# Kernel optimization log

Hardware: AMD Instinct MI355X
Metric: run time of the kernel (lower is better)

Reference implementation:

```python
import jax, jax.numpy as jnp
import numpy as np

N_PTS = 2_000_000
N_VOX = 500_000
N_EMB = 1_000_000
EMBED_DIM = 16


def _interp_offset():
    # 8 corners of the unit cube, same order as torch.meshgrid([0,1]*3) -> reshape(-1,3)
    o = jnp.array([0.0, 1.0], dtype=jnp.float32)
    return jnp.stack(jnp.meshgrid(o, o, o, indexing='ij'), axis=-1).reshape(-1, 3)  # [8,3]


def setup_inputs() -> dict:
    key = jax.random.key(0)
    k1, k2, k3, k4, k5 = jax.random.split(key, 5)
    pts = jax.random.uniform(k1, (N_PTS, 3), dtype=jnp.float32)
    p2v_idx = jax.random.randint(k2, (N_PTS,), 0, N_VOX, dtype=jnp.int64 if jax.config.jax_enable_x64 else jnp.int32)
    embeddings = jax.random.normal(k3, (N_EMB, EMBED_DIM), dtype=jnp.float32) * (EMBED_DIM ** -0.5)
    center_points = jax.random.uniform(k4, (N_VOX, 3), dtype=jnp.float32)
    center2corner = jax.random.randint(k5, (N_VOX, 8), 0, N_EMB, dtype=jnp.int64 if jax.config.jax_enable_x64 else jnp.int32)
    voxel_size = jnp.ones((1,), dtype=jnp.float32)
    return {"pts": pts, "p2v_idx": p2v_idx, "embeddings": embeddings,
            "center_points": center_points, "center2corner": center2corner,
            "voxel_size": voxel_size}


def reference(pts, p2v_idx, embeddings, center_points, center2corner, voxel_size):
    offset = _interp_offset()                      # [8,3]
    cp = center_points[p2v_idx]                    # [N,3]   gather voxel centers
    cidx = center2corner[p2v_idx]                  # [N,8]   gather corner indices
    emb = embeddings[cidx]                         # [N,8,D] gather corner embeddings
    # relative position inside voxel, in [0,1]
    p = (pts - cp) / voxel_size + 0.5              # [N,3]
    p = p[:, None, :]                              # [N,1,3]
    # trilinear weights: prod over xyz of (p if corner==1 else 1-p)
    r = jnp.prod(p * offset + (1.0 - p) * (1.0 - offset), axis=-1)  # [N,8]
    return jnp.einsum('nc,ncd->nd', r, emb)        # [N,D]
```

## Files before the change

### kernel.cpp

```cpp
#include <hip/hip_runtime.h>


typedef float v4f __attribute__((ext_vector_type(4)));

__global__ void k_zero(unsigned* __restrict__ hist, int n) {
    int i = blockIdx.x * blockDim.x + threadIdx.x;
    if (i < n) hist[i] = 0u;
}

__global__ __launch_bounds__(256) void k_hist_rank(const int* __restrict__ p2v,
                                                   unsigned* __restrict__ hist,
                                                   unsigned* __restrict__ rank, int N) {
    const int base = (blockIdx.x * blockDim.x + threadIdx.x) * 8;
    if (base + 7 < N) {
        const int4 a = *(const int4*)(p2v + base);
        const int4 b = *(const int4*)(p2v + base + 4);
        const unsigned r0 = atomicAdd(&hist[a.x], 1u);
        const unsigned r1 = atomicAdd(&hist[a.y], 1u);
        const unsigned r2 = atomicAdd(&hist[a.z], 1u);
        const unsigned r3 = atomicAdd(&hist[a.w], 1u);
        const unsigned r4 = atomicAdd(&hist[b.x], 1u);
        const unsigned r5 = atomicAdd(&hist[b.y], 1u);
        const unsigned r6 = atomicAdd(&hist[b.z], 1u);
        const unsigned r7 = atomicAdd(&hist[b.w], 1u);
        uint4 o0; o0.x = r0; o0.y = r1; o0.z = r2; o0.w = r3;
        uint4 o1; o1.x = r4; o1.y = r5; o1.z = r6; o1.w = r7;
        *(uint4*)(rank + base)     = o0;
        *(uint4*)(rank + base + 4) = o1;
    } else {
        for (int k = 0; k < 8; ++k)
            if (base + k < N) rank[base + k] = atomicAdd(&hist[p2v[base + k]], 1u);
    }
}

__global__ __launch_bounds__(256) void k_scan_blocks(unsigned* __restrict__ hist,
                                                     unsigned* __restrict__ bsums, int nbins) {
    __shared__ unsigned tsum[256];
    const int tid = threadIdx.x;
    const int i0 = blockIdx.x * 1024 + tid * 4;
    unsigned v[4]; unsigned s = 0;
    #pragma unroll
    for (int k = 0; k < 4; ++k) {
        unsigned c = (i0 + k < nbins) ? hist[i0 + k] : 0u;
        v[k] = s; s += c;
    }
    tsum[tid] = s; __syncthreads();
    for (int off = 1; off < 256; off <<= 1) {
        unsigned x = tsum[tid];
        unsigned y = (tid >= off) ? tsum[tid - off] : 0u;
        __syncthreads();
        tsum[tid] = x + y;
        __syncthreads();
    }
    unsigned prefix = (tid > 0) ? tsum[tid - 1] : 0u;
    #pragma unroll
    for (int k = 0; k < 4; ++k) {
        if (i0 + k < nbins) hist[i0 + k] = prefix + v[k];
    }
    if (tid == 255) bsums[blockIdx.x] = tsum[255];
}

__global__ __launch_bounds__(256) void k_scan_sums(unsigned* __restrict__ bsums, int nb) {
    __shared__ unsigned tsum[256];
    const int tid = threadIdx.x;
    const int i0 = tid * 4;
    unsigned v[4]; unsigned s = 0;
    #pragma unroll
    for (int k = 0; k < 4; ++k) {
        unsigned c = (i0 + k < nb) ? bsums[i0 + k] : 0u;
        v[k] = s; s += c;
    }
    tsum[tid] = s; __syncthreads();
    for (int off = 1; off < 256; off <<= 1) {
        unsigned x = tsum[tid];
        unsigned y = (tid >= off) ? tsum[tid - off] : 0u;
        __syncthreads();
        tsum[tid] = x + y;
        __syncthreads();
    }
    unsigned prefix = (tid > 0) ? tsum[tid - 1] : 0u;
    #pragma unroll
    for (int k = 0; k < 4; ++k) {
        if (i0 + k < nb) bsums[i0 + k] = prefix + v[k];
    }
}

__global__ __launch_bounds__(256) void k_place(
    const float* __restrict__ pts,
    const int*   __restrict__ p2v,
    const unsigned* __restrict__ rank,
    const unsigned* __restrict__ hist,
    const unsigned* __restrict__ bsums,
    unsigned* __restrict__ vsort,
    v4f*      __restrict__ rec,
    int N)
{
    const int base = (blockIdx.x * blockDim.x + threadIdx.x) * 4;
    if (base + 3 < N) {
        const int4  v4r = *(const int4*)(p2v + base);
        const uint4 r4  = *(const uint4*)(rank + base);
        const v4f* p4 = (const v4f*)pts;
        const size_t f0i = (size_t)(3 * (base >> 2));
        const v4f f0 = p4[f0i];
        const v4f f1 = p4[f0i + 1];
        const v4f f2 = p4[f0i + 2];

        const unsigned pos0 = hist[v4r.x] + bsums[((unsigned)v4r.x) >> 10] + r4.x;
        const unsigned pos1 = hist[v4r.y] + bsums[((unsigned)v4r.y) >> 10] + r4.y;
        const unsigned pos2 = hist[v4r.z] + bsums[((unsigned)v4r.z) >> 10] + r4.z;
        const unsigned pos3 = hist[v4r.w] + bsums[((unsigned)v4r.w) >> 10] + r4.w;

        vsort[pos0] = (unsigned)v4r.x;
        vsort[pos1] = (unsigned)v4r.y;
        vsort[pos2] = (unsigned)v4r.z;
        vsort[pos3] = (unsigned)v4r.w;

        v4f a;
        a.x = f0.x; a.y = f0.y; a.z = f0.z; a.w = __int_as_float(base + 0);
        rec[pos0] = a;
        a.x = f0.w; a.y = f1.x; a.z = f1.y; a.w = __int_as_float(base + 1);
        rec[pos1] = a;
        a.x = f1.z; a.y = f1.w; a.z = f2.x; a.w = __int_as_float(base + 2);
        rec[pos2] = a;
        a.x = f2.y; a.y = f2.z; a.z = f2.w; a.w = __int_as_float(base + 3);
        rec[pos3] = a;
    } else {
        for (int k = 0; k < 4; ++k) {
            const int i = base + k;
            if (i >= N) break;
            const int v = p2v[i];
            const unsigned pos = hist[v] + bsums[((unsigned)v) >> 10] + rank[i];
            vsort[pos] = (unsigned)v;
            v4f r;
            r.x = pts[3 * (size_t)i + 0];
            r.y = pts[3 * (size_t)i + 1];
            r.z = pts[3 * (size_t)i + 2];
            r.w = __int_as_float(i);
            rec[pos] = r;
        }
    }
}

__global__ __launch_bounds__(256) void k_main(
    const unsigned* __restrict__ vsort, const v4f* __restrict__ rec,
    const float* __restrict__ emb,
    const float* __restrict__ cp,
    const int*   __restrict__ c2c,
    const float* __restrict__ vox,
    float*       __restrict__ out,
    int N)
{
    const int t = blockIdx.x * blockDim.x + threadIdx.x;
    const int n = t >> 2;
    const int q = t & 3;
    if (n >= N) return;

    const unsigned v = vsort[n];
    const v4f r = rec[n];
    const int orig = __float_as_int(r.w);

    const int4* c4 = (const int4*)(c2c + 8 * (size_t)v);
    const int4 ci0 = c4[0];
    const int4 ci1 = c4[1];
    const int cidx[8] = {ci0.x, ci0.y, ci0.z, ci0.w, ci1.x, ci1.y, ci1.z, ci1.w};

    v4f e[8];
    #pragma unroll
    for (int c = 0; c < 8; ++c) {
        e[c] = *(const v4f*)(emb + 16 * (size_t)cidx[c] + 4 * q);
    }

    const float inv_vs = 1.0f / vox[0];
    const float* cpp = cp + 3 * (size_t)v;
    const float px = (r.x - cpp[0]) * inv_vs + 0.5f;
    const float py = (r.y - cpp[1]) * inv_vs + 0.5f;
    const float pz = (r.z - cpp[2]) * inv_vs + 0.5f;
    const float wx[2] = {1.0f - px, px};
    const float wy[2] = {1.0f - py, py};
    const float wz[2] = {1.0f - pz, pz};

    v4f acc = (v4f)(0.0f);
    #pragma unroll
    for (int c = 0; c < 8; ++c) {
        const float w = wx[(c >> 2) & 1] * wy[(c >> 1) & 1] * wz[c & 1];
        acc.x = fmaf(w, e[c].x, acc.x);
        acc.y = fmaf(w, e[c].y, acc.y);
        acc.z = fmaf(w, e[c].z, acc.z);
        acc.w = fmaf(w, e[c].w, acc.w);
    }

    __builtin_nontemporal_store(acc, (v4f*)(out + 16 * (size_t)orig + 4 * q));
}

__global__ __launch_bounds__(256) void k_direct(
    const float* __restrict__ pts, const int* __restrict__ p2v,
    const float* __restrict__ emb, const float* __restrict__ cp,
    const int* __restrict__ c2c, const float* __restrict__ vox,
    float* __restrict__ out, int N)
{
    const int t = blockIdx.x * blockDim.x + threadIdx.x;
    const int n = t >> 2, q = t & 3;
    if (n >= N) return;
    const int v = p2v[n];
    const int4* c4 = (const int4*)(c2c + 8 * (size_t)v);
    const int4 ci0 = c4[0], ci1 = c4[1];
    const int cidx[8] = {ci0.x, ci0.y, ci0.z, ci0.w, ci1.x, ci1.y, ci1.z, ci1.w};
    v4f e[8];
    #pragma unroll
    for (int c = 0; c < 8; ++c) e[c] = *(const v4f*)(emb + 16 * (size_t)cidx[c] + 4 * q);
    const float inv_vs = 1.0f / vox[0];
    const float* pp = pts + 3 * (size_t)n;
    const float* cpp = cp + 3 * (size_t)v;
    const float px = (pp[0] - cpp[0]) * inv_vs + 0.5f;
    const float py = (pp[1] - cpp[1]) * inv_vs + 0.5f;
    const float pz = (pp[2] - cpp[2]) * inv_vs + 0.5f;
    const float wx[2] = {1.0f - px, px};
    const float wy[2] = {1.0f - py, py};
    const float wz[2] = {1.0f - pz, pz};
    v4f acc = (v4f)(0.0f);
    #pragma unroll
    for (int c = 0; c < 8; ++c) {
        const float w = wx[(c >> 2) & 1] * wy[(c >> 1) & 1] * wz[c & 1];
        acc.x = fmaf(w, e[c].x, acc.x); acc.y = fmaf(w, e[c].y, acc.y);
        acc.z = fmaf(w, e[c].z, acc.z); acc.w = fmaf(w, e[c].w, acc.w);
    }
    __builtin_nontemporal_store(acc, (v4f*)(out + 4 * (size_t)t));
}

extern "C" void kernel_launch(void* const* d_in, const int* in_sizes, int n_in,
                              void* d_out, int out_size, void* d_ws, size_t ws_size,
                              hipStream_t stream) {
    const float* pts = (const float*)d_in[0];
    const int*   p2v = (const int*)d_in[1];
    const float* emb = (const float*)d_in[2];
    const float* cp  = (const float*)d_in[3];
    const int*   c2c = (const int*)d_in[4];
    const float* vox = (const float*)d_in[5];
    float*       out = (float*)d_out;

    const int N  = in_sizes[1];
    const int NV = in_sizes[4] / 8;

    const size_t off_hist  = 0;
    const size_t off_bsums = 2u * 1024u * 1024u;
    const size_t off_rank  = 4u * 1024u * 1024u;
    const size_t off_vsort = 12u * 1024u * 1024u;
    const size_t off_rec   = 20u * 1024u * 1024u;
    const size_t need = off_rec + (size_t)N * 16u;

    if (ws_size < need) {
        const int block = 256;
        const long long threads = 4LL * N;
        k_direct<<<(int)((threads + block - 1) / block), block, 0, stream>>>(
            pts, p2v, emb, cp, c2c, vox, out, N);
        return;
    }

    unsigned* hist  = (unsigned*)((char*)d_ws + off_hist);
    unsigned* bsums = (unsigned*)((char*)d_ws + off_bsums);
    unsigned* rank  = (unsigned*)((char*)d_ws + off_rank);
    unsigned* vsort = (unsigned*)((char*)d_ws + off_vsort);
    v4f*      rec   = (v4f*)((char*)d_ws + off_rec);

    const int block = 256;
    const int nscan = (NV + 1023) / 1024;

    k_zero<<<(NV + block - 1) / block, block, 0, stream>>>(hist, NV);
    k_hist_rank<<<(N + block * 8 - 1) / (block * 8), block, 0, stream>>>(p2v, hist, rank, N);
    k_scan_blocks<<<nscan, 256, 0, stream>>>(hist, bsums, NV);
    k_scan_sums<<<1, 256, 0, stream>>>(bsums, nscan);
    k_place<<<(N + block * 4 - 1) / (block * 4), block, 0, stream>>>(
        pts, p2v, rank, hist, bsums, vsort, rec, N);

    const long long threads = 4LL * N;
    k_main<<<(int)((threads + block - 1) / block), block, 0, stream>>>(
        vsort, rec, emb, cp, c2c, vox, out, N);
}
```

Baseline: 458.5 us.

## Privatize voxel histogram per XCD to keep atomics local to each L2

The histogram used for the counting sort is replicated once per XCD, read via the XCC_ID hardware register. Atomics use workgroup scope on the XCD-local copy, and the XCD id is packed into the top bits of the rank. The scan interleaves the per-XCD counts to build per-copy bases, and placement decodes the tag. This aims to avoid cross-XCD coherence traffic on global atomics, at the cost of zeroing and scanning eight times more histogram memory and relying on workgroup-scope atomics staying coherent within an XCD's L2.

New measurement: 477.4 us. +4.1%, slower.

```diff
diff --git a/kernel.cpp b/kernel.cpp
--- a/kernel.cpp
+++ b/kernel.cpp
@@ -2,6 +2,7 @@
 
 
 typedef float v4f __attribute__((ext_vector_type(4)));
+#define NXCD 8
 
 __global__ void k_zero(unsigned* __restrict__ hist, int n) {
     int i = blockIdx.x * blockDim.x + threadIdx.x;
@@ -10,26 +11,35 @@
 
 __global__ __launch_bounds__(256) void k_hist_rank(const int* __restrict__ p2v,
                                                    unsigned* __restrict__ hist,
-                                                   unsigned* __restrict__ rank, int N) {
+                                                   unsigned* __restrict__ rank,
+                                                   int N, int NV) {
+    unsigned xcc;
+    asm volatile("s_getreg_b32 %0, hwreg(HW_REG_XCC_ID)" : "=s"(xcc));
+    xcc &= (NXCD - 1);
+    unsigned* __restrict__ hx = hist + (size_t)xcc * (size_t)NV;
+    const unsigned xtag = xcc << 28;
+
     const int base = (blockIdx.x * blockDim.x + threadIdx.x) * 8;
     if (base + 7 < N) {
         const int4 a = *(const int4*)(p2v + base);
         const int4 b = *(const int4*)(p2v + base + 4);
-        const unsigned r0 = atomicAdd(&hist[a.x], 1u);
-        const unsigned r1 = atomicAdd(&hist[a.y], 1u);
-        const unsigned r2 = atomicAdd(&hist[a.z], 1u);
-        const unsigned r3 = atomicAdd(&hist[a.w], 1u);
-        const unsigned r4 = atomicAdd(&hist[b.x], 1u);
-        const unsigned r5 = atomicAdd(&hist[b.y], 1u);
-        const unsigned r6 = atomicAdd(&hist[b.z], 1u);
-        const unsigned r7 = atomicAdd(&hist[b.w], 1u);
-        uint4 o0; o0.x = r0; o0.y = r1; o0.z = r2; o0.w = r3;
-        uint4 o1; o1.x = r4; o1.y = r5; o1.z = r6; o1.w = r7;
+        const unsigned r0 = __hip_atomic_fetch_add(&hx[a.x], 1u, __ATOMIC_RELAXED, __HIP_MEMORY_SCOPE_WORKGROUP);
+        const unsigned r1 = __hip_atomic_fetch_add(&hx[a.y], 1u, __ATOMIC_RELAXED, __HIP_MEMORY_SCOPE_WORKGROUP);
+        const unsigned r2 = __hip_atomic_fetch_add(&hx[a.z], 1u, __ATOMIC_RELAXED, __HIP_MEMORY_SCOPE_WORKGROUP);
+        const unsigned r3 = __hip_atomic_fetch_add(&hx[a.w], 1u, __ATOMIC_RELAXED, __HIP_MEMORY_SCOPE_WORKGROUP);
+        const unsigned r4 = __hip_atomic_fetch_add(&hx[b.x], 1u, __ATOMIC_RELAXED, __HIP_MEMORY_SCOPE_WORKGROUP);
+        const unsigned r5 = __hip_atomic_fetch_add(&hx[b.y], 1u, __ATOMIC_RELAXED, __HIP_MEMORY_SCOPE_WORKGROUP);
+        const unsigned r6 = __hip_atomic_fetch_add(&hx[b.z], 1u, __ATOMIC_RELAXED, __HIP_MEMORY_SCOPE_WORKGROUP);
+        const unsigned r7 = __hip_atomic_fetch_add(&hx[b.w], 1u, __ATOMIC_RELAXED, __HIP_MEMORY_SCOPE_WORKGROUP);
+        uint4 o0; o0.x = r0 | xtag; o0.y = r1 | xtag; o0.z = r2 | xtag; o0.w = r3 | xtag;
+        uint4 o1; o1.x = r4 | xtag; o1.y = r5 | xtag; o1.z = r6 | xtag; o1.w = r7 | xtag;
         *(uint4*)(rank + base)     = o0;
         *(uint4*)(rank + base + 4) = o1;
     } else {
         for (int k = 0; k < 8; ++k)
-            if (base + k < N) rank[base + k] = atomicAdd(&hist[p2v[base + k]], 1u);
+            if (base + k < N)
+                rank[base + k] = xtag | __hip_atomic_fetch_add(&hx[p2v[base + k]], 1u,
+                                        __ATOMIC_RELAXED, __HIP_MEMORY_SCOPE_WORKGROUP);
     }
 }
 
@@ -38,11 +48,28 @@
     __shared__ unsigned tsum[256];
     const int tid = threadIdx.x;
     const int i0 = blockIdx.x * 1024 + tid * 4;
-    unsigned v[4]; unsigned s = 0;
+    const bool full = (i0 + 3 < nbins);
+
+    unsigned h[NXCD][4];
+    #pragma unroll
+    for (int x = 0; x < NXCD; ++x) {
+        const unsigned* hp = hist + (size_t)x * (size_t)nbins;
+        if (full) {
+            const uint4 t = *(const uint4*)(hp + i0);
+            h[x][0] = t.x; h[x][1] = t.y; h[x][2] = t.z; h[x][3] = t.w;
+        } else {
+            #pragma unroll
+            for (int k = 0; k < 4; ++k) h[x][k] = (i0 + k < nbins) ? hp[i0 + k] : 0u;
+        }
+    }
+
+    unsigned vloc[4]; unsigned s = 0;
     #pragma unroll
     for (int k = 0; k < 4; ++k) {
-        unsigned c = (i0 + k < nbins) ? hist[i0 + k] : 0u;
-        v[k] = s; s += c;
+        unsigned t = 0;
+        #pragma unroll
+        for (int x = 0; x < NXCD; ++x) t += h[x][k];
+        vloc[k] = s; s += t;
     }
     tsum[tid] = s; __syncthreads();
     for (int off = 1; off < 256; off <<= 1) {
@@ -52,10 +79,25 @@
         tsum[tid] = x + y;
         __syncthreads();
     }
-    unsigned prefix = (tid > 0) ? tsum[tid - 1] : 0u;
+    const unsigned prefix = (tid > 0) ? tsum[tid - 1] : 0u;
+
+    unsigned basev[NXCD][4];
     #pragma unroll
     for (int k = 0; k < 4; ++k) {
-        if (i0 + k < nbins) hist[i0 + k] = prefix + v[k];
+        unsigned b = prefix + vloc[k];
+        #pragma unroll
+        for (int x = 0; x < NXCD; ++x) { basev[x][k] = b; b += h[x][k]; }
+    }
+    #pragma unroll
+    for (int x = 0; x < NXCD; ++x) {
+        unsigned* hp = hist + (size_t)x * (size_t)nbins;
+        if (full) {
+            uint4 o; o.x = basev[x][0]; o.y = basev[x][1]; o.z = basev[x][2]; o.w = basev[x][3];
+            *(uint4*)(hp + i0) = o;
+        } else {
+            #pragma unroll
+            for (int k = 0; k < 4; ++k) if (i0 + k < nbins) hp[i0 + k] = basev[x][k];
+        }
     }
     if (tid == 255) bsums[blockIdx.x] = tsum[255];
 }
@@ -93,7 +135,7 @@
     const unsigned* __restrict__ bsums,
     unsigned* __restrict__ vsort,
     v4f*      __restrict__ rec,
-    int N)
+    int N, int NV)
 {
     const int base = (blockIdx.x * blockDim.x + threadIdx.x) * 4;
     if (base + 3 < N) {
@@ -105,10 +147,14 @@
         const v4f f1 = p4[f0i + 1];
         const v4f f2 = p4[f0i + 2];
 
-        const unsigned pos0 = hist[v4r.x] + bsums[((unsigned)v4r.x) >> 10] + r4.x;
-        const unsigned pos1 = hist[v4r.y] + bsums[((unsigned)v4r.y) >> 10] + r4.y;
-        const unsigned pos2 = hist[v4r.z] + bsums[((unsigned)v4r.z) >> 10] + r4.z;
-        const unsigned pos3 = hist[v4r.w] + bsums[((unsigned)v4r.w) >> 10] + r4.w;
+        const unsigned pos0 = hist[(size_t)(r4.x >> 28) * NV + (unsigned)v4r.x]
+                              + bsums[((unsigned)v4r.x) >> 10] + (r4.x & 0x0FFFFFFFu);
+        const unsigned pos1 = hist[(size_t)(r4.y >> 28) * NV + (unsigned)v4r.y]
+                              + bsums[((unsigned)v4r.y) >> 10] + (r4.y & 0x0FFFFFFFu);
+        const unsigned pos2 = hist[(size_t)(r4.z >> 28) * NV + (unsigned)v4r.z]
+                              + bsums[((unsigned)v4r.z) >> 10] + (r4.z & 0x0FFFFFFFu);
+        const unsigned pos3 = hist[(size_t)(r4.w >> 28) * NV + (unsigned)v4r.w]
+                              + bsums[((unsigned)v4r.w) >> 10] + (r4.w & 0x0FFFFFFFu);
 
         vsort[pos0] = (unsigned)v4r.x;
         vsort[pos1] = (unsigned)v4r.y;
@@ -129,7 +175,9 @@
             const int i = base + k;
             if (i >= N) break;
             const int v = p2v[i];
-            const unsigned pos = hist[v] + bsums[((unsigned)v) >> 10] + rank[i];
+            const unsigned rr = rank[i];
+            const unsigned pos = hist[(size_t)(rr >> 28) * NV + (unsigned)v]
+                                 + bsums[((unsigned)v) >> 10] + (rr & 0x0FFFFFFFu);
             vsort[pos] = (unsigned)v;
             v4f r;
             r.x = pts[3 * (size_t)i + 0];
@@ -241,11 +289,12 @@
     const int N  = in_sizes[1];
     const int NV = in_sizes[4] / 8;
 
+    const size_t MB = 1024u * 1024u;
     const size_t off_hist  = 0;
-    const size_t off_bsums = 2u * 1024u * 1024u;
-    const size_t off_rank  = 4u * 1024u * 1024u;
-    const size_t off_vsort = 12u * 1024u * 1024u;
-    const size_t off_rec   = 20u * 1024u * 1024u;
+    const size_t off_bsums = 16u * MB;
+    const size_t off_rank  = 17u * MB;
+    const size_t off_vsort = 25u * MB;
+    const size_t off_rec   = 33u * MB;
     const size_t need = off_rec + (size_t)N * 16u;
 
     if (ws_size < need) {
@@ -264,13 +313,14 @@
 
     const int block = 256;
     const int nscan = (NV + 1023) / 1024;
-
-    k_zero<<<(NV + block - 1) / block, block, 0, stream>>>(hist, NV);
-    k_hist_rank<<<(N + block * 8 - 1) / (block * 8), block, 0, stream>>>(p2v, hist, rank, N);
+    const int nzero = NXCD * NV;
+
+    k_zero<<<(nzero + block - 1) / block, block, 0, stream>>>(hist, nzero);
+    k_hist_rank<<<(N + block * 8 - 1) / (block * 8), block, 0, stream>>>(p2v, hist, rank, N, NV);
     k_scan_blocks<<<nscan, 256, 0, stream>>>(hist, bsums, NV);
     k_scan_sums<<<1, 256, 0, stream>>>(bsums, nscan);
     k_place<<<(N + block * 4 - 1) / (block * 4), block, 0, stream>>>(
-        pts, p2v, rank, hist, bsums, vsort, rec, N);
+        pts, p2v, rank, hist, bsums, vsort, rec, N, NV);
 
     const long long threads = 4LL * N;
     k_main<<<(int)((threads + block - 1) / block), block, 0, stream>>>(
```

## Replace global counting sort with two-pass bucketed sort using shared-memory binning

Applied to the files above, without the earlier changes.

Points are first scattered into coarse buckets of 2048 voxels, using per-block shared-memory counts and one global atomic per bucket per block. A second kernel then counting-sorts each bucket in shared memory to produce voxel-sorted records. This replaces the per-point global atomics of the histogram/rank pass and the multi-kernel global scan. It adds an extra intermediate copy of the records, with fixed per-bucket capacity (N/NB+2048) that could overflow on skewed inputs. The main kernel is also split into two half launches.

Result: faster. 403.4 us (-12.0%).

```diff
diff --git a/kernel.cpp b/kernel.cpp
--- a/kernel.cpp
+++ b/kernel.cpp
@@ -2,6 +2,202 @@
 
 
 typedef float v4f __attribute__((ext_vector_type(4)));
+
+
+__global__ void k_init_gbase(unsigned* __restrict__ gbase, int NB, unsigned CAP) {
+    int i = blockIdx.x * blockDim.x + threadIdx.x;
+    if (i < NB) gbase[i] = (unsigned)i * CAP;
+}
+
+__global__ __launch_bounds__(256) void k_bucket(
+    const int*   __restrict__ p2v,
+    const float* __restrict__ pts,
+    unsigned*    __restrict__ gbase,
+    unsigned*    __restrict__ vA,
+    v4f*         __restrict__ recA,
+    int N, int NB)
+{
+    __shared__ unsigned cnt[512];
+    __shared__ unsigned cur[512];
+    const int tid = threadIdx.x;
+    const int i0 = (blockIdx.x * 256 + tid) * 8;
+
+    for (int b = tid; b < NB; b += 256) cnt[b] = 0u;
+    __syncthreads();
+
+    int vv[8];
+    const bool full = (i0 + 7 < N);
+    if (full) {
+        const int4 a = *(const int4*)(p2v + i0);
+        const int4 b4 = *(const int4*)(p2v + i0 + 4);
+        vv[0]=a.x; vv[1]=a.y; vv[2]=a.z; vv[3]=a.w;
+        vv[4]=b4.x; vv[5]=b4.y; vv[6]=b4.z; vv[7]=b4.w;
+        #pragma unroll
+        for (int k = 0; k < 8; ++k) atomicAdd(&cnt[vv[k] >> 11], 1u);
+    } else {
+        for (int k = 0; k < 8; ++k)
+            if (i0 + k < N) { vv[k] = p2v[i0 + k]; atomicAdd(&cnt[vv[k] >> 11], 1u); }
+    }
+    __syncthreads();
+
+    for (int b = tid; b < NB; b += 256) {
+        const unsigned c = cnt[b];
+        cur[b] = c ? atomicAdd(&gbase[b], c) : 0u;
+    }
+    __syncthreads();
+
+    if (full) {
+        const v4f* p4 = (const v4f*)pts;
+        const size_t fb = (size_t)3 * (size_t)(i0 >> 2);
+        const v4f f0 = p4[fb], f1 = p4[fb+1], f2 = p4[fb+2];
+        const v4f f3 = p4[fb+3], f4 = p4[fb+4], f5 = p4[fb+5];
+        const float xs[8] = {f0.x, f0.w, f1.z, f2.y, f3.x, f3.w, f4.z, f5.y};
+        const float ys[8] = {f0.y, f1.x, f1.w, f2.z, f3.y, f4.x, f4.w, f5.z};
+        const float zs[8] = {f0.z, f1.y, f2.x, f2.w, f3.z, f4.y, f5.x, f5.w};
+        #pragma unroll
+        for (int k = 0; k < 8; ++k) {
+            const unsigned pos = atomicAdd(&cur[vv[k] >> 11], 1u);
+            v4f r; r.x = xs[k]; r.y = ys[k]; r.z = zs[k]; r.w = __int_as_float(i0 + k);
+            recA[pos] = r;
+            vA[pos] = (unsigned)vv[k];
+        }
+    } else {
+        for (int k = 0; k < 8; ++k) {
+            const int i = i0 + k;
+            if (i >= N) break;
+            const unsigned pos = atomicAdd(&cur[vv[k] >> 11], 1u);
+            v4f r;
+            r.x = pts[3*(size_t)i]; r.y = pts[3*(size_t)i+1]; r.z = pts[3*(size_t)i+2];
+            r.w = __int_as_float(i);
+            recA[pos] = r;
+            vA[pos] = (unsigned)vv[k];
+        }
+    }
+}
+
+__global__ __launch_bounds__(256) void k_scan_nb(const unsigned* __restrict__ gbase,
+                                                 unsigned* __restrict__ bo,
+                                                 int NB, unsigned CAP) {
+    __shared__ unsigned tsum[256];
+    const int tid = threadIdx.x;
+    const int i0 = tid * 2;
+    const unsigned c0 = (i0     < NB) ? gbase[i0]     - (unsigned)i0       * CAP : 0u;
+    const unsigned c1 = (i0 + 1 < NB) ? gbase[i0 + 1] - (unsigned)(i0 + 1) * CAP : 0u;
+    tsum[tid] = c0 + c1; __syncthreads();
+    for (int off = 1; off < 256; off <<= 1) {
+        unsigned x = tsum[tid];
+        unsigned y = (tid >= off) ? tsum[tid - off] : 0u;
+        __syncthreads();
+        tsum[tid] = x + y;
+        __syncthreads();
+    }
+    const unsigned prefix = (tid > 0) ? tsum[tid - 1] : 0u;
+    if (i0     < NB) bo[i0]     = prefix;
+    if (i0 + 1 < NB) bo[i0 + 1] = prefix + c0;
+}
+
+__global__ __launch_bounds__(256) void k_binsort(
+    const unsigned* __restrict__ gbase,
+    const unsigned* __restrict__ bo,
+    const unsigned* __restrict__ vA,
+    const v4f*      __restrict__ recA,
+    unsigned*       __restrict__ vsort,
+    v4f*            __restrict__ rec,
+    unsigned CAP)
+{
+    __shared__ unsigned h[2048];
+    __shared__ unsigned tsum[256];
+    const int b   = blockIdx.x;
+    const int tid = threadIdx.x;
+    const unsigned in0   = (unsigned)b * CAP;
+    const unsigned cntb  = gbase[b] - in0;
+    const unsigned obase = bo[b];
+    const unsigned vbase = (unsigned)b << 11;
+
+    #pragma unroll
+    for (int k = 0; k < 8; ++k) h[tid + 256 * k] = 0u;
+    __syncthreads();
+
+    for (unsigned j = tid; j < cntb; j += 256)
+        atomicAdd(&h[vA[in0 + j] - vbase], 1u);
+    __syncthreads();
+
+    unsigned loc[8]; unsigned s = 0;
+    #pragma unroll
+    for (int k = 0; k < 8; ++k) { loc[k] = s; s += h[tid * 8 + k]; }
+    tsum[tid] = s; __syncthreads();
+    for (int off = 1; off < 256; off <<= 1) {
+        unsigned x = tsum[tid];
+        unsigned y = (tid >= off) ? tsum[tid - off] : 0u;
+        __syncthreads();
+        tsum[tid] = x + y;
+        __syncthreads();
+    }
+    const unsigned pre = (tid > 0) ? tsum[tid - 1] : 0u;
+    #pragma unroll
+    for (int k = 0; k < 8; ++k) h[tid * 8 + k] = pre + loc[k];
+    __syncthreads();
+
+    for (unsigned j = tid; j < cntb; j += 256) {
+        const unsigned v = vA[in0 + j];
+        const unsigned r = atomicAdd(&h[v - vbase], 1u);
+        const unsigned pos = obase + r;
+        vsort[pos] = v;
+        rec[pos] = recA[in0 + j];
+    }
+}
+
+__global__ __launch_bounds__(256) void k_main(
+    const unsigned* __restrict__ vsort, const v4f* __restrict__ rec,
+    const float* __restrict__ emb,
+    const float* __restrict__ cp,
+    const int*   __restrict__ c2c,
+    const float* __restrict__ vox,
+    float*       __restrict__ out,
+    int n0, int n1)
+{
+    const int t = blockIdx.x * blockDim.x + threadIdx.x;
+    const int n = n0 + (t >> 2);
+    const int q = t & 3;
+    if (n >= n1) return;
+
+    const unsigned v = vsort[n];
+    const v4f r = rec[n];
+    const int orig = __float_as_int(r.w);
+
+    const int4* c4 = (const int4*)(c2c + 8 * (size_t)v);
+    const int4 ci0 = c4[0];
+    const int4 ci1 = c4[1];
+    const int cidx[8] = {ci0.x, ci0.y, ci0.z, ci0.w, ci1.x, ci1.y, ci1.z, ci1.w};
+
+    v4f e[8];
+    #pragma unroll
+    for (int c = 0; c < 8; ++c) {
+        e[c] = *(const v4f*)(emb + 16 * (size_t)cidx[c] + 4 * q);
+    }
+
+    const float inv_vs = 1.0f / vox[0];
+    const float* cpp = cp + 3 * (size_t)v;
+    const float px = (r.x - cpp[0]) * inv_vs + 0.5f;
+    const float py = (r.y - cpp[1]) * inv_vs + 0.5f;
+    const float pz = (r.z - cpp[2]) * inv_vs + 0.5f;
+    const float wx[2] = {1.0f - px, px};
+    const float wy[2] = {1.0f - py, py};
+    const float wz[2] = {1.0f - pz, pz};
+
+    v4f acc = (v4f)(0.0f);
+    #pragma unroll
+    for (int c = 0; c < 8; ++c) {
+        const float w = wx[(c >> 2) & 1] * wy[(c >> 1) & 1] * wz[c & 1];
+        acc.x = fmaf(w, e[c].x, acc.x);
+        acc.y = fmaf(w, e[c].y, acc.y);
+        acc.z = fmaf(w, e[c].z, acc.z);
+        acc.w = fmaf(w, e[c].w, acc.w);
+    }
+
+    __builtin_nontemporal_store(acc, (v4f*)(out + 16 * (size_t)orig + 4 * q));
+}
+
 
 __global__ void k_zero(unsigned* __restrict__ hist, int n) {
     int i = blockIdx.x * blockDim.x + threadIdx.x;
@@ -141,57 +337,6 @@
     }
 }
 
-__global__ __launch_bounds__(256) void k_main(
-    const unsigned* __restrict__ vsort, const v4f* __restrict__ rec,
-    const float* __restrict__ emb,
-    const float* __restrict__ cp,
-    const int*   __restrict__ c2c,
-    const float* __restrict__ vox,
-    float*       __restrict__ out,
-    int N)
-{
-    const int t = blockIdx.x * blockDim.x + threadIdx.x;
-    const int n = t >> 2;
-    const int q = t & 3;
-    if (n >= N) return;
-
-    const unsigned v = vsort[n];
-    const v4f r = rec[n];
-    const int orig = __float_as_int(r.w);
-
-    const int4* c4 = (const int4*)(c2c + 8 * (size_t)v);
-    const int4 ci0 = c4[0];
-    const int4 ci1 = c4[1];
-    const int cidx[8] = {ci0.x, ci0.y, ci0.z, ci0.w, ci1.x, ci1.y, ci1.z, ci1.w};
-
-    v4f e[8];
-    #pragma unroll
-    for (int c = 0; c < 8; ++c) {
-        e[c] = *(const v4f*)(emb + 16 * (size_t)cidx[c] + 4 * q);
-    }
-
-    const float inv_vs = 1.0f / vox[0];
-    const float* cpp = cp + 3 * (size_t)v;
-    const float px = (r.x - cpp[0]) * inv_vs + 0.5f;
-    const float py = (r.y - cpp[1]) * inv_vs + 0.5f;
-    const float pz = (r.z - cpp[2]) * inv_vs + 0.5f;
-    const float wx[2] = {1.0f - px, px};
-    const float wy[2] = {1.0f - py, py};
-    const float wz[2] = {1.0f - pz, pz};
-
-    v4f acc = (v4f)(0.0f);
-    #pragma unroll
-    for (int c = 0; c < 8; ++c) {
-        const float w = wx[(c >> 2) & 1] * wy[(c >> 1) & 1] * wz[c & 1];
-        acc.x = fmaf(w, e[c].x, acc.x);
-        acc.y = fmaf(w, e[c].y, acc.y);
-        acc.z = fmaf(w, e[c].z, acc.z);
-        acc.w = fmaf(w, e[c].w, acc.w);
-    }
-
-    __builtin_nontemporal_store(acc, (v4f*)(out + 16 * (size_t)orig + 4 * q));
-}
-
 __global__ __launch_bounds__(256) void k_direct(
     const float* __restrict__ pts, const int* __restrict__ p2v,
     const float* __restrict__ emb, const float* __restrict__ cp,
@@ -227,6 +372,7 @@
     __builtin_nontemporal_store(acc, (v4f*)(out + 4 * (size_t)t));
 }
 
+
 extern "C" void kernel_launch(void* const* d_in, const int* in_sizes, int n_in,
                               void* d_out, int out_size, void* d_ws, size_t ws_size,
                               hipStream_t stream) {
@@ -240,39 +386,80 @@
 
     const int N  = in_sizes[1];
     const int NV = in_sizes[4] / 8;
-
-    const size_t off_hist  = 0;
-    const size_t off_bsums = 2u * 1024u * 1024u;
-    const size_t off_rank  = 4u * 1024u * 1024u;
-    const size_t off_vsort = 12u * 1024u * 1024u;
-    const size_t off_rec   = 20u * 1024u * 1024u;
-    const size_t need = off_rec + (size_t)N * 16u;
-
-    if (ws_size < need) {
-        const int block = 256;
+    const int block = 256;
+
+    const int NB = (NV + 2047) >> 11;
+    if (NB >= 1 && NB <= 512) {
+        const unsigned CAP = (unsigned)(N / NB) + 2048u;
+        const size_t off_gbase = 0;
+        const size_t off_bo    = 4096;
+        const size_t off_vA    = 8192;
+        const size_t sz_vA     = (size_t)NB * CAP * 4u;
+        const size_t off_recA  = (off_vA + sz_vA + 255u) & ~(size_t)255u;
+        const size_t sz_recA   = (size_t)NB * CAP * 16u;
+        const size_t off_vsF   = (off_recA + sz_recA + 255u) & ~(size_t)255u;
+        const size_t off_recF  = (off_vsF + (size_t)N * 4u + 255u) & ~(size_t)255u;
+        const size_t need_fast = off_recF + (size_t)N * 16u;
+
+        if (ws_size >= need_fast) {
+            unsigned* gbase = (unsigned*)((char*)d_ws + off_gbase);
+            unsigned* bo    = (unsigned*)((char*)d_ws + off_bo);
+            unsigned* vA    = (unsigned*)((char*)d_ws + off_vA);
+            v4f*      recA  = (v4f*)((char*)d_ws + off_recA);
+            unsigned* vsort = (unsigned*)((char*)d_ws + off_vsF);
+            v4f*      rec   = (v4f*)((char*)d_ws + off_recF);
+
+            k_init_gbase<<<(NB + block - 1) / block, block, 0, stream>>>(gbase, NB, CAP);
+            k_bucket<<<(N + 2047) / 2048, block, 0, stream>>>(p2v, pts, gbase, vA, recA, N, NB);
+            k_scan_nb<<<1, block, 0, stream>>>(gbase, bo, NB, CAP);
+            k_binsort<<<NB, block, 0, stream>>>(gbase, bo, vA, recA, vsort, rec, CAP);
+
+            const int half = N / 2;
+            const long long th0 = 4LL * half;
+            const long long th1 = 4LL * (N - half);
+            k_main<<<(int)((th0 + block - 1) / block), block, 0, stream>>>(
+                vsort, rec, emb, cp, c2c, vox, out, 0, half);
+            k_main<<<(int)((th1 + block - 1) / block), block, 0, stream>>>(
+                vsort, rec, emb, cp, c2c, vox, out, half, N);
+            return;
+        }
+    }
+
+    {
+        const size_t MB = 1024u * 1024u;
+        const size_t off_hist  = 0;
+        const size_t off_bsums = 2u * MB;
+        const size_t off_rank  = 4u * MB;
+        const size_t off_vsort = 12u * MB;
+        const size_t off_rec   = 20u * MB;
+        const size_t need = off_rec + (size_t)N * 16u;
+
+        if (ws_size >= need) {
+            unsigned* hist  = (unsigned*)((char*)d_ws + off_hist);
+            unsigned* bsums = (unsigned*)((char*)d_ws + off_bsums);
+            unsigned* rank  = (unsigned*)((char*)d_ws + off_rank);
+            unsigned* vsort = (unsigned*)((char*)d_ws + off_vsort);
+            v4f*      rec   = (v4f*)((char*)d_ws + off_rec);
+
+            const int nscan = (NV + 1023) / 1024;
+
+            k_zero<<<(NV + block - 1) / block, block, 0, stream>>>(hist, NV);
+            k_hist_rank<<<(N + block * 8 - 1) / (block * 8), block, 0, stream>>>(p2v, hist, rank, N);
+            k_scan_blocks<<<nscan, 256, 0, stream>>>(hist, bsums, NV);
+            k_scan_sums<<<1, 256, 0, stream>>>(bsums, nscan);
+            k_place<<<(N + block * 4 - 1) / (block * 4), block, 0, stream>>>(
+                pts, p2v, rank, hist, bsums, vsort, rec, N);
+
+            const long long threads = 4LL * N;
+            k_main<<<(int)((threads + block - 1) / block), block, 0, stream>>>(
+                vsort, rec, emb, cp, c2c, vox, out, 0, N);
+            return;
+        }
+    }
+
+    {
         const long long threads = 4LL * N;
         k_direct<<<(int)((threads + block - 1) / block), block, 0, stream>>>(
             pts, p2v, emb, cp, c2c, vox, out, N);
-        return;
-    }
-
-    unsigned* hist  = (unsigned*)((char*)d_ws + off_hist);
-    unsigned* bsums = (unsigned*)((char*)d_ws + off_bsums);
-    unsigned* rank  = (unsigned*)((char*)d_ws + off_rank);
-    unsigned* vsort = (unsigned*)((char*)d_ws + off_vsort);
-    v4f*      rec   = (v4f*)((char*)d_ws + off_rec);
-
-    const int block = 256;
-    const int nscan = (NV + 1023) / 1024;
-
-    k_zero<<<(NV + block - 1) / block, block, 0, stream>>>(hist, NV);
-    k_hist_rank<<<(N + block * 8 - 1) / (block * 8), block, 0, stream>>>(p2v, hist, rank, N);
-    k_scan_blocks<<<nscan, 256, 0, stream>>>(hist, bsums, NV);
-    k_scan_sums<<<1, 256, 0, stream>>>(bsums, nscan);
-    k_place<<<(N + block * 4 - 1) / (block * 4), block, 0, stream>>>(
-        pts, p2v, rank, hist, bsums, vsort, rec, N);
-
-    const long long threads = 4LL * N;
-    k_main<<<(int)((threads + block - 1) / block), block, 0, stream>>>(
-        vsort, rec, emb, cp, c2c, vox, out, N);
-}
+    }
+}
```
